# Performance work log

Measured on AMD Instinct MI355X. Metric: run time of the kernel, lower is better.

## Reference

```python
import jax, jax.numpy as jnp
import numpy as np

B, S, E, H = 8, 1024, 768, 12
D = E // H  # 64


def setup_inputs() -> dict:
    key = jax.random.key(0)
    ks = jax.random.split(key, 9)
    s = 0.02
    hidden_state = jax.random.normal(ks[0], (B, S, E), dtype=jnp.float32)
    # per-head projections stacked: [H, E, D]
    Wq = jax.random.normal(ks[1], (H, E, D), dtype=jnp.float32) * s
    Wk = jax.random.normal(ks[2], (H, E, D), dtype=jnp.float32) * s
    Wv = jax.random.normal(ks[3], (H, E, D), dtype=jnp.float32) * s
    bq = jax.random.normal(ks[4], (H, D), dtype=jnp.float32) * s
    bk = jax.random.normal(ks[5], (H, D), dtype=jnp.float32) * s
    bv = jax.random.normal(ks[6], (H, D), dtype=jnp.float32) * s
    Wo = jax.random.normal(ks[7], (E, E), dtype=jnp.float32) * s
    bo = jax.random.normal(ks[8], (E,), dtype=jnp.float32) * s
    return dict(hidden_state=hidden_state, Wq=Wq, Wk=Wk, Wv=Wv,
                bq=bq, bk=bk, bv=bv, Wo=Wo, bo=bo)


def reference(hidden_state, Wq, Wk, Wv, bq, bk, bv, Wo, bo):
    # project: [B,S,E] x [H,E,D] -> [B,H,S,D]
    q = jnp.einsum('bse,hed->bhsd', hidden_state, Wq) + bq[None, :, None, :]
    k = jnp.einsum('bse,hed->bhsd', hidden_state, Wk) + bk[None, :, None, :]
    v = jnp.einsum('bse,hed->bhsd', hidden_state, Wv) + bv[None, :, None, :]
    scale = 1.0 / jnp.sqrt(jnp.float32(D))
    scores = jnp.einsum('bhsd,bhtd->bhst', q, k) * scale  # [B,H,S,S]
    weights = jax.nn.softmax(scores, axis=-1)
    attn = jnp.einsum('bhst,bhtd->bhsd', weights, v)  # [B,H,S,D]
    # concat heads -> [B,S,E]
    x = attn.transpose(0, 2, 1, 3).reshape(B, S, E)
    return x @ Wo + bo
```

## Files before the change

kernel.cpp:

```cpp
#include <hip/hip_runtime.h>
#include <math.h>

#define BB 8
#define SS 1024
#define EE 768
#define HH 12
#define DD 64

typedef short bf16x8 __attribute__((ext_vector_type(8)));
typedef float f32x4  __attribute__((ext_vector_type(4)));
typedef unsigned short u16x8 __attribute__((ext_vector_type(8)));

__device__ __forceinline__ unsigned short f2bf(float f) {
    union { float f; unsigned u; } v; v.f = f;
    unsigned r = v.u + 0x7fffu + ((v.u >> 16) & 1u);
    return (unsigned short)(r >> 16);
}

#define SWZ(row, byte) ((byte) ^ (((row) & 7) << 4))

__global__ __launch_bounds__(256) void conv_hs_kernel(
    const float* __restrict__ in, unsigned short* __restrict__ out)
{
    size_t i = ((size_t)blockIdx.x * 256 + threadIdx.x) * 8;
    float4 a = *reinterpret_cast<const float4*>(&in[i]);
    float4 b = *reinterpret_cast<const float4*>(&in[i + 4]);
    u16x8 o;
    o[0] = f2bf(a.x); o[1] = f2bf(a.y); o[2] = f2bf(a.z); o[3] = f2bf(a.w);
    o[4] = f2bf(b.x); o[5] = f2bf(b.y); o[6] = f2bf(b.z); o[7] = f2bf(b.w);
    *reinterpret_cast<u16x8*>(&out[i]) = o;
}

__global__ __launch_bounds__(256) void conv_wqkv_kernel(
    const float* __restrict__ Wq, const float* __restrict__ Wk,
    const float* __restrict__ Wv, unsigned short* __restrict__ WT)
{
    const int z = blockIdx.z;
    const int which = z / HH, h = z - which * HH;
    const float* in = ((which == 0) ? Wq : (which == 1) ? Wk : Wv) + (size_t)h * EE * DD;
    unsigned short* out = WT + (size_t)z * DD * EE;
    const float sc = (which == 0) ? 0.125f : 1.0f;

    __shared__ float t[64][65];
    const int tid = threadIdx.x;
    const int rt0 = blockIdx.x * 64;

    #pragma unroll
    for (int i = 0; i < 16; ++i) {
        int lin = tid + i * 256;
        int r = lin >> 6, c = lin & 63;
        t[r][c] = in[(size_t)(rt0 + r) * DD + c];
    }
    __syncthreads();
    #pragma unroll
    for (int i = 0; i < 16; ++i) {
        int lin = tid + i * 256;
        int c = lin >> 6, r = lin & 63;
        out[(size_t)c * EE + rt0 + r] = f2bf(t[r][c] * sc);
    }
}

__global__ __launch_bounds__(256) void conv_wo_kernel(
    const float* __restrict__ Wo, unsigned short* __restrict__ WoT)
{
    __shared__ float t[64][65];
    const int tid = threadIdx.x;
    const int rt0 = blockIdx.x * 64;
    const int ct0 = blockIdx.y * 64;

    #pragma unroll
    for (int i = 0; i < 16; ++i) {
        int lin = tid + i * 256;
        int r = lin >> 6, c = lin & 63;
        t[r][c] = Wo[(size_t)(rt0 + r) * EE + ct0 + c];
    }
    __syncthreads();
    #pragma unroll
    for (int i = 0; i < 16; ++i) {
        int lin = tid + i * 256;
        int c = lin >> 6, r = lin & 63;
        WoT[(size_t)(ct0 + c) * EE + rt0 + r] = f2bf(t[r][c]);
    }
}

__global__ __launch_bounds__(256) void qkv_mfma_kernel(
    const unsigned short* __restrict__ hsb, const unsigned short* __restrict__ WT,
    const float* __restrict__ bq, const float* __restrict__ bk, const float* __restrict__ bv,
    unsigned short* __restrict__ qo, unsigned short* __restrict__ ko,
    unsigned short* __restrict__ vto)
{
    __shared__ alignas(16) char As[128 * 128];
    __shared__ alignas(16) char Bs[128 * 128];

    const int tid = threadIdx.x;
    const int wv  = tid >> 6;
    const int ln  = tid & 63;
    const int g   = ln >> 4;
    const int lr  = ln & 15;
    const int wr  = wv >> 1;
    const int wc  = wv & 1;
    const int r0  = blockIdx.x * 128;
    const int c0  = blockIdx.y * 128;

    f32x4 acc[4][4] = {};

    for (int k0 = 0; k0 < EE; k0 += 64) {
        __syncthreads();
        #pragma unroll
        for (int i = 0; i < 4; ++i) {
            int seg = tid + i * 256;
            int row = seg >> 3;
            int ch  = seg & 7;
            *reinterpret_cast<bf16x8*>(As + SWZ(row, row * 128 + ch * 16)) =
                *reinterpret_cast<const bf16x8*>(&hsb[(size_t)(r0 + row) * EE + k0 + ch * 8]);
            *reinterpret_cast<bf16x8*>(Bs + SWZ(row, row * 128 + ch * 16)) =
                *reinterpret_cast<const bf16x8*>(&WT[(size_t)(c0 + row) * EE + k0 + ch * 8]);
        }
        __syncthreads();

        #pragma unroll
        for (int c = 0; c < 2; ++c) {
            bf16x8 af[4];
            #pragma unroll
            for (int m = 0; m < 4; ++m) {
                const int arow = wr * 64 + m * 16 + lr;
                af[m] = *reinterpret_cast<const bf16x8*>(
                    As + SWZ(arow, arow * 128 + c * 64 + g * 16));
            }
            #pragma unroll
            for (int nf = 0; nf < 4; ++nf) {
                const int bcol = wc * 64 + nf * 16 + lr;
                bf16x8 bf = *reinterpret_cast<const bf16x8*>(
                    Bs + SWZ(bcol, bcol * 128 + c * 64 + g * 16));
                #pragma unroll
                for (int m = 0; m < 4; ++m)
                    acc[m][nf] = __builtin_amdgcn_mfma_f32_16x16x32_bf16(af[m], bf, acc[m][nf], 0, 0, 0);
            }
        }
    }

    const int zz    = (c0 + wc * 64) >> 6;
    const int which = zz / HH;
    const int h     = zz - which * HH;
    const float* bias = (which == 0) ? bq : (which == 1) ? bk : bv;
    const float bsc   = (which == 0) ? 0.125f : 1.0f;

    if (which < 2) {
        unsigned short* C = (which == 0) ? qo : ko;
        #pragma unroll
        for (int nf = 0; nf < 4; ++nf) {
            const int d = nf * 16 + lr;
            const float bia = bias[h * DD + d] * bsc;
            #pragma unroll
            for (int m = 0; m < 4; ++m)
                #pragma unroll
                for (int rr = 0; rr < 4; ++rr) {
                    int row = r0 + wr * 64 + m * 16 + g * 4 + rr;
                    int b_ = row >> 10, s_ = row & 1023;
                    C[((size_t)(b_ * HH + h) * SS + s_) * DD + d] = f2bf(acc[m][nf][rr] + bia);
                }
        }
    } else {
        #pragma unroll
        for (int nf = 0; nf < 4; ++nf) {
            const int d = nf * 16 + lr;
            const float bia = bias[h * DD + d];
            #pragma unroll
            for (int m = 0; m < 4; ++m)
                #pragma unroll
                for (int rr = 0; rr < 4; ++rr) {
                    int row = r0 + wr * 64 + m * 16 + g * 4 + rr;
                    int b_ = row >> 10, s_ = row & 1023;
                    vto[((size_t)(b_ * HH + h) * DD + d) * SS + s_] = f2bf(acc[m][nf][rr] + bia);
                }
        }
    }
}

__global__ __launch_bounds__(256) void attn_mfma_kernel(
    const unsigned short* __restrict__ qb, const unsigned short* __restrict__ kb,
    const unsigned short* __restrict__ vtb, unsigned short* __restrict__ x)
{
    __shared__ alignas(16) char Ks[64 * 128];
    __shared__ alignas(16) char Vs[64 * 128];
    __shared__ alignas(16) char Pl[4 * 32 * 128];

    const int tid = threadIdx.x;
    const int wv  = tid >> 6;
    const int ln  = tid & 63;
    const int g   = ln >> 4;
    const int lr  = ln & 15;

    const int id = blockIdx.x;
    const int xc = id & 7;
    const int j  = id >> 3;
    const int bh = xc * 12 + (j >> 3);
    const int qx = j & 7;
    const int qw = qx * 128 + wv * 32;

    bf16x8 qf[2][2];
    #pragma unroll
    for (int w = 0; w < 2; ++w) {
        const size_t qr = (size_t)(bh * SS + qw + w * 16 + lr) * DD;
        qf[w][0] = *reinterpret_cast<const bf16x8*>(&qb[qr + g * 8]);
        qf[w][1] = *reinterpret_cast<const bf16x8*>(&qb[qr + 32 + g * 8]);
    }

    f32x4 acc_o[2][4] = {};
    f32x4 lrow[2] = {};

    char* Pw = Pl + wv * 4096;

    for (int t0 = 0; t0 < SS; t0 += 64) {
        __syncthreads();
        #pragma unroll
        for (int i = 0; i < 2; ++i) {
            int c = tid + i * 256;
            int row = c >> 3;
            int seg = c & 7;
            *reinterpret_cast<bf16x8*>(Ks + SWZ(row, row * 128 + seg * 16)) =
                *reinterpret_cast<const bf16x8*>(&kb[(size_t)(bh * SS + t0 + row) * DD + seg * 8]);
            *reinterpret_cast<bf16x8*>(Vs + SWZ(row, row * 128 + seg * 16)) =
                *reinterpret_cast<const bf16x8*>(&vtb[(size_t)(bh * DD + row) * SS + t0 + seg * 8]);
        }
        __syncthreads();

        f32x4 s[2][4] = {};
        #pragma unroll
        for (int kf = 0; kf < 4; ++kf) {
            const int key = kf * 16 + lr;
            bf16x8 k0 = *reinterpret_cast<const bf16x8*>(Ks + SWZ(key, key * 128 + g * 16));
            bf16x8 k1 = *reinterpret_cast<const bf16x8*>(Ks + SWZ(key, key * 128 + 64 + g * 16));
            #pragma unroll
            for (int w = 0; w < 2; ++w) {
                s[w][kf] = __builtin_amdgcn_mfma_f32_16x16x32_bf16(qf[w][0], k0, s[w][kf], 0, 0, 0);
                s[w][kf] = __builtin_amdgcn_mfma_f32_16x16x32_bf16(qf[w][1], k1, s[w][kf], 0, 0, 0);
            }
        }

        #pragma unroll
        for (int w = 0; w < 2; ++w)
            #pragma unroll
            for (int kf = 0; kf < 4; ++kf)
                #pragma unroll
                for (int r = 0; r < 4; ++r) {
                    float p = __expf(s[w][kf][r]);
                    lrow[w][r] += p;
                    int row = w * 16 + g * 4 + r;
                    *reinterpret_cast<unsigned short*>(
                        Pw + SWZ(row, row * 128 + (kf * 16 + lr) * 2)) = f2bf(p);
                }

        #pragma unroll
        for (int kk = 0; kk < 2; ++kk) {
            bf16x8 pf[2];
            #pragma unroll
            for (int w = 0; w < 2; ++w) {
                const int prow = w * 16 + lr;
                pf[w] = *reinterpret_cast<const bf16x8*>(
                    Pw + SWZ(prow, prow * 128 + kk * 64 + g * 16));
            }
            #pragma unroll
            for (int nf = 0; nf < 4; ++nf) {
                const int d = nf * 16 + lr;
                bf16x8 vf = *reinterpret_cast<const bf16x8*>(
                    Vs + SWZ(d, d * 128 + kk * 64 + g * 16));
                #pragma unroll
                for (int w = 0; w < 2; ++w)
                    acc_o[w][nf] = __builtin_amdgcn_mfma_f32_16x16x32_bf16(pf[w], vf, acc_o[w][nf], 0, 0, 0);
            }
        }
    }

    #pragma unroll
    for (int off = 1; off <= 8; off <<= 1)
        #pragma unroll
        for (int w = 0; w < 2; ++w)
            #pragma unroll
            for (int r = 0; r < 4; ++r) lrow[w][r] += __shfl_xor(lrow[w][r], off, 64);

    const int b_ = bh / HH;
    const int h_ = bh % HH;
    #pragma unroll
    for (int w = 0; w < 2; ++w)
        #pragma unroll
        for (int nf = 0; nf < 4; ++nf)
            #pragma unroll
            for (int r = 0; r < 4; ++r) {
                x[(size_t)(b_ * SS + qw + w * 16 + g * 4 + r) * EE + h_ * DD + nf * 16 + lr] =
                    f2bf(acc_o[w][nf][r] / lrow[w][r]);
            }
}

__global__ __launch_bounds__(256) void out_mfma_kernel(
    const unsigned short* __restrict__ xb, const unsigned short* __restrict__ WoT,
    const float* __restrict__ bo, float* __restrict__ out)
{
    __shared__ alignas(16) char As[128 * 128];
    __shared__ alignas(16) char Bs[128 * 128];

    const int tid = threadIdx.x;
    const int wv  = tid >> 6;
    const int ln  = tid & 63;
    const int g   = ln >> 4;
    const int lr  = ln & 15;
    const int wr  = wv >> 1;
    const int wc  = wv & 1;
    const int r0  = blockIdx.x * 128;
    const int c0  = blockIdx.y * 128;

    f32x4 acc[4][4] = {};

    for (int k0 = 0; k0 < EE; k0 += 64) {
        __syncthreads();
        #pragma unroll
        for (int i = 0; i < 4; ++i) {
            int seg = tid + i * 256;
            int row = seg >> 3;
            int ch  = seg & 7;
            *reinterpret_cast<bf16x8*>(As + SWZ(row, row * 128 + ch * 16)) =
                *reinterpret_cast<const bf16x8*>(&xb[(size_t)(r0 + row) * EE + k0 + ch * 8]);
            *reinterpret_cast<bf16x8*>(Bs + SWZ(row, row * 128 + ch * 16)) =
                *reinterpret_cast<const bf16x8*>(&WoT[(size_t)(c0 + row) * EE + k0 + ch * 8]);
        }
        __syncthreads();

        #pragma unroll
        for (int c = 0; c < 2; ++c) {
            bf16x8 af[4];
            #pragma unroll
            for (int m = 0; m < 4; ++m) {
                const int arow = wr * 64 + m * 16 + lr;
                af[m] = *reinterpret_cast<const bf16x8*>(
                    As + SWZ(arow, arow * 128 + c * 64 + g * 16));
            }
            #pragma unroll
            for (int nf = 0; nf < 4; ++nf) {
                const int bcol = wc * 64 + nf * 16 + lr;
                bf16x8 bf = *reinterpret_cast<const bf16x8*>(
                    Bs + SWZ(bcol, bcol * 128 + c * 64 + g * 16));
                #pragma unroll
                for (int m = 0; m < 4; ++m)
                    acc[m][nf] = __builtin_amdgcn_mfma_f32_16x16x32_bf16(af[m], bf, acc[m][nf], 0, 0, 0);
            }
        }
    }

    #pragma unroll
    for (int nf = 0; nf < 4; ++nf) {
        const int col = c0 + wc * 64 + nf * 16 + lr;
        const float bia = bo[col];
        #pragma unroll
        for (int m = 0; m < 4; ++m)
            #pragma unroll
            for (int rr = 0; rr < 4; ++rr) {
                int row = r0 + wr * 64 + m * 16 + g * 4 + rr;
                out[(size_t)row * EE + col] = acc[m][nf][rr] + bia;
            }
    }
}

extern "C" void kernel_launch(void* const* d_in, const int* in_sizes, int n_in,
                              void* d_out, int out_size, void* d_ws, size_t ws_size,
                              hipStream_t stream) {
    const float* hs = (const float*)d_in[0];
    const float* Wq = (const float*)d_in[1];
    const float* Wk = (const float*)d_in[2];
    const float* Wv = (const float*)d_in[3];
    const float* bq = (const float*)d_in[4];
    const float* bk = (const float*)d_in[5];
    const float* bv = (const float*)d_in[6];
    const float* Wo = (const float*)d_in[7];
    const float* bo = (const float*)d_in[8];
    float* out = (float*)d_out;

    const size_t per = (size_t)BB * HH * SS * DD;
    unsigned short* qb  = (unsigned short*)d_ws;
    unsigned short* kb  = qb + per;
    unsigned short* vtb = kb + per;
    unsigned short* xb  = vtb + per;
    unsigned short* hsb = xb + per;
    unsigned short* WT  = hsb + per;
    unsigned short* WoT = WT + (size_t)3 * HH * DD * EE;

    conv_hs_kernel<<<dim3(BB * SS * EE / 8 / 256), 256, 0, stream>>>(hs, hsb);
    conv_wqkv_kernel<<<dim3(EE / 64, 1, 3 * HH), 256, 0, stream>>>(Wq, Wk, Wv, WT);
    conv_wo_kernel<<<dim3(EE / 64, EE / 64), 256, 0, stream>>>(Wo, WoT);

    qkv_mfma_kernel<<<dim3(BB * SS / 128, 3 * HH * DD / 128), 256, 0, stream>>>(
        hsb, WT, bq, bk, bv, qb, kb, vtb);

    attn_mfma_kernel<<<dim3((SS / 128) * BB * HH), 256, 0, stream>>>(qb, kb, vtb, xb);

    out_mfma_kernel<<<dim3(BB * SS / 128, EE / 128), 256, 0, stream>>>(xb, WoT, bo, out);
}
```

Measured before the change: 229.1 us.

## Use direct global-to-LDS loads and double-buffer K/V tiles in attention

Replaces the register-staged global-to-shared copies in the QKV projection GEMM, the output projection GEMM and the attention kernel with global_load_lds 16-byte DMA loads. The XOR swizzle is kept by permuting which source chunk each lane fetches. The attention kernel also double-buffers its K and V tiles, so it issues the next tile's loads before computing on the current one and needs only one barrier per iteration. This is meant to cut VGPR traffic and hide global latency, at the cost of twice the K/V shared memory and a reliance on the barrier to wait for the async loads.

```diff
diff --git a/kernel.cpp b/kernel.cpp
--- a/kernel.cpp
+++ b/kernel.cpp
@@ -18,6 +18,12 @@
 }
 
 #define SWZ(row, byte) ((byte) ^ (((row) & 7) << 4))
+
+__device__ __forceinline__ void ldsload16(const void* g, void* l) {
+    __builtin_amdgcn_global_load_lds(
+        (const __attribute__((address_space(1))) void*)g,
+        (__attribute__((address_space(3))) void*)l, 16, 0, 0);
+}
 
 __global__ __launch_bounds__(256) void conv_hs_kernel(
     const float* __restrict__ in, unsigned short* __restrict__ out)
@@ -108,13 +114,12 @@
         __syncthreads();
         #pragma unroll
         for (int i = 0; i < 4; ++i) {
-            int seg = tid + i * 256;
-            int row = seg >> 3;
-            int ch  = seg & 7;
-            *reinterpret_cast<bf16x8*>(As + SWZ(row, row * 128 + ch * 16)) =
-                *reinterpret_cast<const bf16x8*>(&hsb[(size_t)(r0 + row) * EE + k0 + ch * 8]);
-            *reinterpret_cast<bf16x8*>(Bs + SWZ(row, row * 128 + ch * 16)) =
-                *reinterpret_cast<const bf16x8*>(&WT[(size_t)(c0 + row) * EE + k0 + ch * 8]);
+            const int seg  = i * 256 + wv * 64 + ln;
+            const int row  = seg >> 3;
+            const int sch  = (seg & 7) ^ (row & 7);
+            const int base = (i * 256 + wv * 64) * 16;
+            ldsload16(&hsb[(size_t)(r0 + row) * EE + k0 + sch * 8], As + base);
+            ldsload16(&WT [(size_t)(c0 + row) * EE + k0 + sch * 8], Bs + base);
         }
         __syncthreads();
 
@@ -181,8 +186,8 @@
     const unsigned short* __restrict__ qb, const unsigned short* __restrict__ kb,
     const unsigned short* __restrict__ vtb, unsigned short* __restrict__ x)
 {
-    __shared__ alignas(16) char Ks[64 * 128];
-    __shared__ alignas(16) char Vs[64 * 128];
+    __shared__ alignas(16) char Ks[2][64 * 128];
+    __shared__ alignas(16) char Vs[2][64 * 128];
     __shared__ alignas(16) char Pl[4 * 32 * 128];
 
     const int tid = threadIdx.x;
@@ -211,26 +216,34 @@
 
     char* Pw = Pl + wv * 4096;
 
-    for (int t0 = 0; t0 < SS; t0 += 64) {
+    auto stage = [&](int buf, int t0) {
+        #pragma unroll
+        for (int i = 0; i < 2; ++i) {
+            const int seg  = i * 256 + wv * 64 + ln;
+            const int row  = seg >> 3;
+            const int sch  = (seg & 7) ^ (row & 7);
+            const int base = (i * 256 + wv * 64) * 16;
+            ldsload16(&kb [(size_t)(bh * SS + t0 + row) * DD + sch * 8], Ks[buf] + base);
+            ldsload16(&vtb[(size_t)(bh * DD + row) * SS + t0 + sch * 8], Vs[buf] + base);
+        }
+    };
+
+    stage(0, 0);
+    int cur = 0;
+
+    for (int tt = 0; tt < SS / 64; ++tt) {
         __syncthreads();
-        #pragma unroll
-        for (int i = 0; i < 2; ++i) {
-            int c = tid + i * 256;
-            int row = c >> 3;
-            int seg = c & 7;
-            *reinterpret_cast<bf16x8*>(Ks + SWZ(row, row * 128 + seg * 16)) =
-                *reinterpret_cast<const bf16x8*>(&kb[(size_t)(bh * SS + t0 + row) * DD + seg * 8]);
-            *reinterpret_cast<bf16x8*>(Vs + SWZ(row, row * 128 + seg * 16)) =
-                *reinterpret_cast<const bf16x8*>(&vtb[(size_t)(bh * DD + row) * SS + t0 + seg * 8]);
-        }
-        __syncthreads();
+        if (tt + 1 < SS / 64) stage(cur ^ 1, (tt + 1) * 64);
+
+        const char* K = Ks[cur];
+        const char* V = Vs[cur];
 
         f32x4 s[2][4] = {};
         #pragma unroll
         for (int kf = 0; kf < 4; ++kf) {
             const int key = kf * 16 + lr;
-            bf16x8 k0 = *reinterpret_cast<const bf16x8*>(Ks + SWZ(key, key * 128 + g * 16));
-            bf16x8 k1 = *reinterpret_cast<const bf16x8*>(Ks + SWZ(key, key * 128 + 64 + g * 16));
+            bf16x8 k0 = *reinterpret_cast<const bf16x8*>(K + SWZ(key, key * 128 + g * 16));
+            bf16x8 k1 = *reinterpret_cast<const bf16x8*>(K + SWZ(key, key * 128 + 64 + g * 16));
             #pragma unroll
             for (int w = 0; w < 2; ++w) {
                 s[w][kf] = __builtin_amdgcn_mfma_f32_16x16x32_bf16(qf[w][0], k0, s[w][kf], 0, 0, 0);
@@ -264,12 +277,13 @@
             for (int nf = 0; nf < 4; ++nf) {
                 const int d = nf * 16 + lr;
                 bf16x8 vf = *reinterpret_cast<const bf16x8*>(
-                    Vs + SWZ(d, d * 128 + kk * 64 + g * 16));
+                    V + SWZ(d, d * 128 + kk * 64 + g * 16));
                 #pragma unroll
                 for (int w = 0; w < 2; ++w)
                     acc_o[w][nf] = __builtin_amdgcn_mfma_f32_16x16x32_bf16(pf[w], vf, acc_o[w][nf], 0, 0, 0);
             }
         }
+        cur ^= 1;
     }
 
     #pragma unroll
@@ -315,13 +329,12 @@
         __syncthreads();
         #pragma unroll
         for (int i = 0; i < 4; ++i) {
-            int seg = tid + i * 256;
-            int row = seg >> 3;
-            int ch  = seg & 7;
-            *reinterpret_cast<bf16x8*>(As + SWZ(row, row * 128 + ch * 16)) =
-                *reinterpret_cast<const bf16x8*>(&xb[(size_t)(r0 + row) * EE + k0 + ch * 8]);
-            *reinterpret_cast<bf16x8*>(Bs + SWZ(row, row * 128 + ch * 16)) =
-                *reinterpret_cast<const bf16x8*>(&WoT[(size_t)(c0 + row) * EE + k0 + ch * 8]);
+            const int seg  = i * 256 + wv * 64 + ln;
+            const int row  = seg >> 3;
+            const int sch  = (seg & 7) ^ (row & 7);
+            const int base = (i * 256 + wv * 64) * 16;
+            ldsload16(&xb [(size_t)(r0 + row) * EE + k0 + sch * 8], As + base);
+            ldsload16(&WoT[(size_t)(c0 + row) * EE + k0 + sch * 8], Bs + base);
         }
         __syncthreads();
 
```

After: 212.1 us. -7.4%, faster.
